# Kernel tuning notes

Hardware: AMD Instinct MI355X
Metric: run time of the kernel (lower is better)

Reference implementation:

```python
import jax, jax.numpy as jnp
import numpy as np

NPOS_MAX = 24  # npos_max
B, HEADS, H, W, HEAD_DIM = 8, 12, 24, 24, 64
SEQ = H * W


def setup_inputs() -> dict:
    key = jax.random.key(0)
    k1, k2, k3, k4 = jax.random.split(key, 4)
    # pos_emb params are zeros in torch init; randomized here so outputs/grads are nontrivial
    return {
        "query": jax.random.normal(k1, (B, HEADS, SEQ, HEAD_DIM), jnp.float32) * 0.1,
        "attn_logits": jax.random.normal(k2, (B, HEADS, SEQ, SEQ), jnp.float32),
        "pos_emb_x": jax.random.normal(k3, (HEAD_DIM, NPOS_MAX), jnp.float32) * 0.02,
        "pos_emb_y": jax.random.normal(k4, (HEAD_DIM, NPOS_MAX), jnp.float32) * 0.02,
        "wx": jnp.float32(0.5),
    }


def _cope_unit(query, attn_logits, pos_emb):
    # query: [N, heads, L, d]; attn_logits: [N, heads, L, L]; pos_emb: [d, npos]
    gates = jax.nn.sigmoid(attn_logits)
    pos = jnp.flip(jnp.cumsum(jnp.flip(gates, -1), axis=-1), -1)
    pos = jnp.minimum(pos, NPOS_MAX - 1)
    pos_ceil = jnp.ceil(pos).astype(jnp.int32)
    pos_floor = jnp.floor(pos).astype(jnp.int32)
    logits_int = jnp.einsum("nhld,dp->nhlp", query, pos_emb)  # [N,heads,L,npos]
    logits_ceil = jnp.take_along_axis(logits_int, pos_ceil, axis=-1)
    logits_floor = jnp.take_along_axis(logits_int, pos_floor, axis=-1)
    w = pos - pos_floor
    return logits_ceil * w + logits_floor * (1.0 - w)  # [N,heads,L,L]


def _cdist(x):
    # x: [BH, N, D] -> pairwise Euclidean distances [BH, N, N] (torch.cdist p=2)
    sq = jnp.sum(x * x, axis=-1)  # [BH, N]
    d2 = sq[:, :, None] + sq[:, None, :] - 2.0 * jnp.einsum("bnd,bmd->bnm", x, x)
    d2 = jnp.maximum(d2, 0.0)
    # safe sqrt: zero (not nan) gradient at identical points, matching torch.cdist
    return jnp.where(d2 > 0, jnp.sqrt(jnp.where(d2 > 0, d2, 1.0)), 0.0)


def reference(query, attn_logits, pos_emb_x, pos_emb_y, wx):
    b, heads, seq, d = query.shape
    h = w = int(np.sqrt(seq))
    q = query.reshape(b, heads, h, w, d)
    # row/column query slices (match torch permutes + reshapes)
    q_x = q.transpose(0, 2, 1, 3, 4).reshape(b * h, heads, w, d)
    q_y = q.transpose(0, 3, 1, 2, 4).reshape(b * w, heads, h, d)

    # vectorized replacement for the nested gather loops
    a = attn_logits.reshape(b, heads, h, w, h, w)
    # attn_x[b,h,i,j,k] = a[b,h,i,j,i,k]  -> diagonal over axes (2,4)
    attn_x = jnp.diagonal(a, axis1=2, axis2=4).transpose(0, 1, 4, 2, 3)  # [B,heads,H,W,W]
    # attn_y[b,h,i,j,k] = a[b,h,j,i,k,i]  -> diagonal over axes (3,5)
    attn_y = jnp.diagonal(a, axis1=3, axis2=5).transpose(0, 1, 4, 2, 3)  # [B,heads,W,H,H]

    # NOTE: faithful to the source's reshape (no permute) of [B,heads,H,W,W] -> [B*H,heads,W,W]
    attn_x_flat = attn_x.reshape(b * h, heads, w, w)
    attn_y_flat = attn_y.reshape(b * w, heads, h, h)

    w_x = _cope_unit(q_x, attn_x_flat, pos_emb_x).reshape(b, h, heads, w, w)
    w_y = _cope_unit(q_y, attn_y_flat, pos_emb_y).reshape(b, w, heads, h, h)

    # get_pe: flatten to [B*heads, H*W, W] / [B*heads, H*W, H] and take pairwise dists
    pe_x_flat = w_x.transpose(0, 2, 1, 3, 4).reshape(b * heads, h * w, w)
    pe_y_flat = w_y.transpose(0, 2, 3, 1, 4).reshape(b * heads, h * w, h)
    pe_res_x = _cdist(pe_x_flat).reshape(b, heads, h * w, h * w)
    pe_res_y = _cdist(pe_y_flat).reshape(b, heads, h * w, h * w)

    return wx * pe_res_x + (1.0 - wx) * pe_res_y
```

## Files before the change

kernel.cpp:

```cpp
#include <hip/hip_runtime.h>
#include <math.h>

#define NH 12
#define S 576
#define DD 64
#define P 24
#define NROWS 55296
#define GELEMS ((long)NROWS * P)
#define PSTRIDE 32

typedef unsigned int uint;
typedef unsigned short ushort;
typedef __bf16 bf16x8 __attribute__((ext_vector_type(8)));
typedef float f32x4 __attribute__((ext_vector_type(4)));

__device__ __forceinline__ uint bf16hi_bits(float v) {
    const uint u = __float_as_uint(v);
    return u + 0x7FFFu + ((u >> 16) & 1u);
}

__global__ __launch_bounds__(256) void gather_kernel(
    const float* __restrict__ attn, float* __restrict__ gx, float* __restrict__ gy)
{
    __shared__ float rb[16][580];
    const int tid = threadIdx.x;
    const int r0 = blockIdx.x * 16;
    const int hd = blockIdx.y, bb = blockIdx.z;
    const float4* src = (const float4*)(attn + ((long)(bb * NH + hd) * S + r0) * S);
    #pragma unroll
    for (int it = 0; it < 9; ++it) {
        const int i = it * 256 + tid;
        const int row = i / 144, c4 = i % 144;
        *(float4*)&rb[row][c4 * 4] = src[i];
    }
    __syncthreads();
    #pragma unroll
    for (int t = 0; t < 3; ++t) {
        const int e = t * 256 + tid;
        const int row = e / 48, jj = e % 48;
        const int r = r0 + row;
        const int band = r / 24, off = r % 24;
        if (jj < 24) {
            gx[((long)((bb * 288 + hd * 24 + band) * 24 + off)) * 24 + jj] =
                rb[row][band * 24 + jj];
        } else {
            const int k = jj - 24;
            gy[((long)((bb * 288 + hd * 24 + off) * 24 + band)) * 24 + k] =
                rb[row][k * 24 + off];
        }
    }
}

__global__ __launch_bounds__(256) void cope_kernel(
    const float* __restrict__ q,
    const float* __restrict__ gx, const float* __restrict__ gy,
    const float* __restrict__ Ex, const float* __restrict__ Ey,
    __bf16* __restrict__ pxh, __bf16* __restrict__ pxl,
    __bf16* __restrict__ pyh, __bf16* __restrict__ pyl,
    float* __restrict__ sqx, float* __restrict__ sqy)
{
    __shared__ float Et[24][68];
    __shared__ float Lr[32][28];
    __shared__ float Wr[32][28];

    const int tid = threadIdx.x;
    const int rl = tid >> 3, j = tid & 7;
    const int gidx0 = blockIdx.x * 32;
    const bool is_y = gidx0 >= NROWS;
    const int gu = gidx0 - (is_y ? NROWS : 0) + rl;

    const int l  = gu % 24;
    const int t2 = gu / 24;
    const int h  = t2 % NH, n = t2 / NH;
    const int bq = n / 24, oq = n % 24;
    const int qr = is_y ? (l * 24 + oq) : (oq * 24 + l);
    const int g  = bq * NH + h;

    const float* E = is_y ? Ey : Ex;
    for (int i = tid; i < 1536; i += 256) {
        const int d = i / 24, p = i % 24;
        Et[p][d] = E[i];
    }
    __syncthreads();

    const float* qrow = q + ((long)g * S + qr) * DD;
    float a0 = 0.f, a1 = 0.f, a2 = 0.f;
    const int p0 = j, p1 = j + 8, p2 = j + 16;
    #pragma unroll
    for (int d4 = 0; d4 < DD; d4 += 4) {
        const float4 qv = *(const float4*)(qrow + d4);
        const float4 e0 = *(const float4*)&Et[p0][d4];
        const float4 e1 = *(const float4*)&Et[p1][d4];
        const float4 e2 = *(const float4*)&Et[p2][d4];
        a0 = fmaf(qv.x, e0.x, fmaf(qv.y, e0.y, fmaf(qv.z, e0.z, fmaf(qv.w, e0.w, a0))));
        a1 = fmaf(qv.x, e1.x, fmaf(qv.y, e1.y, fmaf(qv.z, e1.z, fmaf(qv.w, e1.w, a1))));
        a2 = fmaf(qv.x, e2.x, fmaf(qv.y, e2.y, fmaf(qv.z, e2.z, fmaf(qv.w, e2.w, a2))));
    }
    Lr[rl][p0] = a0; Lr[rl][p1] = a1; Lr[rl][p2] = a2;
    __syncthreads();

    const float* grow = (is_y ? gy : gx) + (long)gu * P + 3 * j;
    float g0 = grow[0], g1 = grow[1], g2 = grow[2];
    g0 = 1.0f / (1.0f + __expf(-g0));
    g1 = 1.0f / (1.0f + __expf(-g1));
    g2 = 1.0f / (1.0f + __expf(-g2));
    const float s = g0 + g1 + g2;
    float T = s;
    #pragma unroll
    for (int d = 1; d < 8; d <<= 1) {
        const float o = __shfl_down(T, d, 8);
        T += (j + d < 8) ? o : 0.0f;
    }
    const float Exc = T - s;
    float posv[3];
    posv[0] = T;
    posv[1] = g1 + g2 + Exc;
    posv[2] = g2 + Exc;

    float sqp = 0.f;
    #pragma unroll
    for (int m = 0; m < 3; ++m) {
        const float pk  = fminf(posv[m], 23.0f);
        const float pf  = floorf(pk);
        const int   ic  = (int)ceilf(pk);
        const int   ifl = (int)pf;
        const float w   = pk - pf;
        const float o   = Lr[rl][ic] * w + Lr[rl][ifl] * (1.0f - w);
        Wr[rl][3 * j + m] = o;
        sqp += o * o;
    }
    #pragma unroll
    for (int d = 1; d < 8; d <<= 1) {
        const float o = __shfl_down(sqp, d, 8);
        sqp += (j + d < 8) ? o : 0.0f;
    }
    if (j == 0) (is_y ? sqy : sqx)[(long)g * S + qr] = sqp;
    __syncthreads();

    const int hl = tid >> 7, rem = tid & 127;
    const int r3 = rem >> 2, seg = rem & 3;
    const int gu3 = gidx0 - (is_y ? NROWS : 0) + r3;
    const int l3 = gu3 % 24, t23 = gu3 / 24;
    const int h3 = t23 % NH, n3 = t23 / NH;
    const int bq3 = n3 / 24, oq3 = n3 % 24;
    const int qr3 = is_y ? (l3 * 24 + oq3) : (oq3 * 24 + l3);
    const int g3 = bq3 * NH + h3;
    __bf16* dst = (is_y ? (hl ? pyl : pyh) : (hl ? pxl : pxh))
                  + ((long)g3 * S + qr3) * PSTRIDE + seg * 8;
    uint pk4[4] = {0u, 0u, 0u, 0u};
    if (seg < 3) {
        ushort hv[8];
        #pragma unroll
        for (int t = 0; t < 8; ++t) {
            const float o = Wr[r3][seg * 8 + t];
            const uint rh = bf16hi_bits(o);
            if (hl == 0) {
                hv[t] = (ushort)(rh >> 16);
            } else {
                const float hif = __uint_as_float(rh & 0xFFFF0000u);
                hv[t] = (ushort)(bf16hi_bits(o - hif) >> 16);
            }
        }
        #pragma unroll
        for (int t = 0; t < 4; ++t)
            pk4[t] = (uint)hv[2 * t] | ((uint)hv[2 * t + 1] << 16);
    }
    *(uint4*)dst = make_uint4(pk4[0], pk4[1], pk4[2], pk4[3]);
}

__global__ __launch_bounds__(256) void dist_kernel(
    const __bf16* __restrict__ pxh, const __bf16* __restrict__ pxl,
    const __bf16* __restrict__ pyh, const __bf16* __restrict__ pyl,
    const float* __restrict__ sqx, const float* __restrict__ sqy,
    const float* __restrict__ wxp, float* __restrict__ out)
{
    const int tid = threadIdx.x;
    const int w = tid >> 6, lane = tid & 63;
    const int til = blockIdx.x * 4 + w;
    if (til >= 81) return;
    const int g = blockIdx.y;
    const int tn = til / 9, tm = til % 9;
    const int lm = lane & 15, kg = lane >> 4;
    const float wx = wxp[0], wyc = 1.0f - wx;
    const long gb = (long)g * S;

    bf16x8 xbh[4], xbl[4], ybh[4], ybl[4];
    float smx[4], smy[4];
    #pragma unroll
    for (int nt = 0; nt < 4; ++nt) {
        const int row = tm * 64 + nt * 16 + lm;
        const long rb = (gb + row) * PSTRIDE + kg * 8;
        xbh[nt] = *(const bf16x8*)(pxh + rb);
        xbl[nt] = *(const bf16x8*)(pxl + rb);
        ybh[nt] = *(const bf16x8*)(pyh + rb);
        ybl[nt] = *(const bf16x8*)(pyl + rb);
        smx[nt] = sqx[gb + row];
        smy[nt] = sqy[gb + row];
    }

    #pragma unroll
    for (int mt = 0; mt < 4; ++mt) {
        const int arow = tn * 64 + mt * 16 + lm;
        const long ra = (gb + arow) * PSTRIDE + kg * 8;
        const bf16x8 xah = *(const bf16x8*)(pxh + ra);
        const bf16x8 xal = *(const bf16x8*)(pxl + ra);
        const bf16x8 yah = *(const bf16x8*)(pyh + ra);
        const bf16x8 yal = *(const bf16x8*)(pyl + ra);
        float snx[4], sny[4];
        #pragma unroll
        for (int rg = 0; rg < 4; ++rg) {
            const int r = tn * 64 + mt * 16 + kg * 4 + rg;
            snx[rg] = sqx[gb + r];
            sny[rg] = sqy[gb + r];
        }
        #pragma unroll
        for (int nt = 0; nt < 4; ++nt) {
            f32x4 ax = {0.f, 0.f, 0.f, 0.f};
            ax = __builtin_amdgcn_mfma_f32_16x16x32_bf16(xah, xbh[nt], ax, 0, 0, 0);
            ax = __builtin_amdgcn_mfma_f32_16x16x32_bf16(xah, xbl[nt], ax, 0, 0, 0);
            ax = __builtin_amdgcn_mfma_f32_16x16x32_bf16(xal, xbh[nt], ax, 0, 0, 0);
            f32x4 ay = {0.f, 0.f, 0.f, 0.f};
            ay = __builtin_amdgcn_mfma_f32_16x16x32_bf16(yah, ybh[nt], ay, 0, 0, 0);
            ay = __builtin_amdgcn_mfma_f32_16x16x32_bf16(yah, ybl[nt], ay, 0, 0, 0);
            ay = __builtin_amdgcn_mfma_f32_16x16x32_bf16(yal, ybh[nt], ay, 0, 0, 0);
            #pragma unroll
            for (int rg = 0; rg < 4; ++rg) {
                const int row = tn * 64 + mt * 16 + kg * 4 + rg;
                const int col = tm * 64 + nt * 16 + lm;
                const float d2x = fmaxf(fmaf(-2.0f, ax[rg], snx[rg] + smx[nt]), 0.0f);
                const float d2y = fmaxf(fmaf(-2.0f, ay[rg], sny[rg] + smy[nt]), 0.0f);
                const float dx = __builtin_amdgcn_sqrtf(d2x);
                const float dy = __builtin_amdgcn_sqrtf(d2y);
                out[(gb + row) * S + col] = fmaf(wx, dx, wyc * dy);
            }
        }
    }
}

extern "C" void kernel_launch(void* const* d_in, const int* in_sizes, int n_in,
                              void* d_out, int out_size, void* d_ws, size_t ws_size,
                              hipStream_t stream) {
    const float* q    = (const float*)d_in[0];
    const float* attn = (const float*)d_in[1];
    const float* Ex   = (const float*)d_in[2];
    const float* Ey   = (const float*)d_in[3];
    const float* wxp  = (const float*)d_in[4];
    float* out = (float*)d_out;

    float* gx = (float*)d_ws;
    float* gy = gx + GELEMS;
    __bf16* pxh = (__bf16*)(gy + GELEMS);
    __bf16* pxl = pxh + (long)NROWS * PSTRIDE;
    __bf16* pyh = pxl + (long)NROWS * PSTRIDE;
    __bf16* pyl = pyh + (long)NROWS * PSTRIDE;
    float* sqx = (float*)(pyl + (long)NROWS * PSTRIDE);
    float* sqy = sqx + NROWS;

    gather_kernel<<<dim3(36, NH, 8), 256, 0, stream>>>(attn, gx, gy);
    cope_kernel<<<3456, 256, 0, stream>>>(q, gx, gy, Ex, Ey,
                                          pxh, pxl, pyh, pyl, sqx, sqy);
    dist_kernel<<<dim3(21, 96), 256, 0, stream>>>(pxh, pxl, pyh, pyl,
                                                  sqx, sqy, wxp, out);
}
```

Before: 281.2 us.

## Fuse attention-logit gather into CoPE kernel, dropping gx/gy intermediates

Removes the separate gather kernel and its gx/gy workspace buffers. The CoPE kernel now loads a 24-row band of attention logits per block, extracts the x and y diagonal gates into shared memory, and handles 24 x-rows plus 24 y-rows per block with 384 threads. This saves one launch and a global write/read round trip of the gathered gates, but makes the gather's index mapping more intricate. The remapping of which rows each block owns must stay exactly equivalent to the original layout.

```diff
diff --git a/kernel.cpp b/kernel.cpp
--- a/kernel.cpp
+++ b/kernel.cpp
@@ -6,7 +6,6 @@
 #define DD 64
 #define P 24
 #define NROWS 55296
-#define GELEMS ((long)NROWS * P)
 #define PSTRIDE 32
 
 typedef unsigned int uint;
@@ -19,69 +18,55 @@
     return u + 0x7FFFu + ((u >> 16) & 1u);
 }
 
-__global__ __launch_bounds__(256) void gather_kernel(
-    const float* __restrict__ attn, float* __restrict__ gx, float* __restrict__ gy)
-{
-    __shared__ float rb[16][580];
-    const int tid = threadIdx.x;
-    const int r0 = blockIdx.x * 16;
-    const int hd = blockIdx.y, bb = blockIdx.z;
-    const float4* src = (const float4*)(attn + ((long)(bb * NH + hd) * S + r0) * S);
-    #pragma unroll
-    for (int it = 0; it < 9; ++it) {
-        const int i = it * 256 + tid;
-        const int row = i / 144, c4 = i % 144;
-        *(float4*)&rb[row][c4 * 4] = src[i];
-    }
-    __syncthreads();
-    #pragma unroll
-    for (int t = 0; t < 3; ++t) {
-        const int e = t * 256 + tid;
-        const int row = e / 48, jj = e % 48;
-        const int r = r0 + row;
-        const int band = r / 24, off = r % 24;
-        if (jj < 24) {
-            gx[((long)((bb * 288 + hd * 24 + band) * 24 + off)) * 24 + jj] =
-                rb[row][band * 24 + jj];
-        } else {
-            const int k = jj - 24;
-            gy[((long)((bb * 288 + hd * 24 + off) * 24 + band)) * 24 + k] =
-                rb[row][k * 24 + off];
-        }
-    }
-}
-
-__global__ __launch_bounds__(256) void cope_kernel(
+__global__ __launch_bounds__(384) void cope_fused_kernel(
     const float* __restrict__ q,
-    const float* __restrict__ gx, const float* __restrict__ gy,
+    const float* __restrict__ attn,
     const float* __restrict__ Ex, const float* __restrict__ Ey,
     __bf16* __restrict__ pxh, __bf16* __restrict__ pxl,
     __bf16* __restrict__ pyh, __bf16* __restrict__ pyl,
     float* __restrict__ sqx, float* __restrict__ sqy)
 {
-    __shared__ float Et[24][68];
-    __shared__ float Lr[32][28];
-    __shared__ float Wr[32][28];
+    __shared__ float Et[2][24][68];
+    __shared__ float xg[24][28];
+    __shared__ float yg[24][25];
+    __shared__ float Lr[48][28];
+    __shared__ float Wr[48][28];
 
     const int tid = threadIdx.x;
+    const int J = blockIdx.x, hd = blockIdx.y, b = blockIdx.z;
+
+    for (int i = tid; i < 3072; i += 384) {
+        const int u = i / 1536, r = i % 1536;
+        Et[u][r % 24][r / 24] = (u ? Ey : Ex)[r];
+    }
+
+    const float4* src = (const float4*)(attn + (((long)(b * NH + hd) * S + J * 24) * S));
+    const int c4lo = 6 * J;
+    #pragma unroll
+    for (int t = 0; t < 9; ++t) {
+        const int i = t * 384 + tid;
+        const int rr = i / 144, c4 = i % 144;
+        const float4 v = src[i];
+        if (c4 >= c4lo && c4 < c4lo + 6) {
+            *(float4*)&xg[rr][(c4 - c4lo) * 4] = v;
+        }
+        const int rem = (c4 * 4) % 24;
+        const int u = (rr - rem + 24) % 24;
+        if (u < 4) {
+            const float sel = (u == 0) ? v.x : (u == 1) ? v.y : (u == 2) ? v.z : v.w;
+            yg[rr][(c4 * 4 + u) / 24] = sel;
+        }
+    }
+    __syncthreads();
+
     const int rl = tid >> 3, j = tid & 7;
-    const int gidx0 = blockIdx.x * 32;
-    const bool is_y = gidx0 >= NROWS;
-    const int gu = gidx0 - (is_y ? NROWS : 0) + rl;
-
-    const int l  = gu % 24;
-    const int t2 = gu / 24;
-    const int h  = t2 % NH, n = t2 / NH;
-    const int bq = n / 24, oq = n % 24;
-    const int qr = is_y ? (l * 24 + oq) : (oq * 24 + l);
-    const int g  = bq * NH + h;
-
-    const float* E = is_y ? Ey : Ex;
-    for (int i = tid; i < 1536; i += 256) {
-        const int d = i / 24, p = i % 24;
-        Et[p][d] = E[i];
-    }
-    __syncthreads();
+    const bool is_y = rl >= 24;
+    const int rr = is_y ? rl - 24 : rl;
+    const int hq = is_y ? (rr % 12) : (J % 12);
+    const int oq = 2 * hd + (is_y ? rr / 12 : J / 12);
+    const int qr = is_y ? (J * 24 + oq) : (oq * 24 + rr);
+    const int g  = b * NH + hq;
+    const int eu = is_y ? 1 : 0;
 
     const float* qrow = q + ((long)g * S + qr) * DD;
     float a0 = 0.f, a1 = 0.f, a2 = 0.f;
@@ -89,9 +74,9 @@
     #pragma unroll
     for (int d4 = 0; d4 < DD; d4 += 4) {
         const float4 qv = *(const float4*)(qrow + d4);
-        const float4 e0 = *(const float4*)&Et[p0][d4];
-        const float4 e1 = *(const float4*)&Et[p1][d4];
-        const float4 e2 = *(const float4*)&Et[p2][d4];
+        const float4 e0 = *(const float4*)&Et[eu][p0][d4];
+        const float4 e1 = *(const float4*)&Et[eu][p1][d4];
+        const float4 e2 = *(const float4*)&Et[eu][p2][d4];
         a0 = fmaf(qv.x, e0.x, fmaf(qv.y, e0.y, fmaf(qv.z, e0.z, fmaf(qv.w, e0.w, a0))));
         a1 = fmaf(qv.x, e1.x, fmaf(qv.y, e1.y, fmaf(qv.z, e1.z, fmaf(qv.w, e1.w, a1))));
         a2 = fmaf(qv.x, e2.x, fmaf(qv.y, e2.y, fmaf(qv.z, e2.z, fmaf(qv.w, e2.w, a2))));
@@ -99,7 +84,7 @@
     Lr[rl][p0] = a0; Lr[rl][p1] = a1; Lr[rl][p2] = a2;
     __syncthreads();
 
-    const float* grow = (is_y ? gy : gx) + (long)gu * P + 3 * j;
+    const float* grow = (is_y ? &yg[rr][0] : &xg[rr][0]) + 3 * j;
     float g0 = grow[0], g1 = grow[1], g2 = grow[2];
     g0 = 1.0f / (1.0f + __expf(-g0));
     g1 = 1.0f / (1.0f + __expf(-g1));
@@ -137,15 +122,15 @@
     if (j == 0) (is_y ? sqy : sqx)[(long)g * S + qr] = sqp;
     __syncthreads();
 
-    const int hl = tid >> 7, rem = tid & 127;
-    const int r3 = rem >> 2, seg = rem & 3;
-    const int gu3 = gidx0 - (is_y ? NROWS : 0) + r3;
-    const int l3 = gu3 % 24, t23 = gu3 / 24;
-    const int h3 = t23 % NH, n3 = t23 / NH;
-    const int bq3 = n3 / 24, oq3 = n3 % 24;
-    const int qr3 = is_y ? (l3 * 24 + oq3) : (oq3 * 24 + l3);
-    const int g3 = bq3 * NH + h3;
-    __bf16* dst = (is_y ? (hl ? pyl : pyh) : (hl ? pxl : pxh))
+    const int hl = tid / 192, rem3 = tid % 192;
+    const int r3 = rem3 >> 2, seg = rem3 & 3;
+    const bool isy3 = r3 >= 24;
+    const int rr3 = isy3 ? r3 - 24 : r3;
+    const int hq3 = isy3 ? (rr3 % 12) : (J % 12);
+    const int oq3 = 2 * hd + (isy3 ? rr3 / 12 : J / 12);
+    const int qr3 = isy3 ? (J * 24 + oq3) : (oq3 * 24 + rr3);
+    const int g3 = b * NH + hq3;
+    __bf16* dst = (isy3 ? (hl ? pyl : pyh) : (hl ? pxl : pxh))
                   + ((long)g3 * S + qr3) * PSTRIDE + seg * 8;
     uint pk4[4] = {0u, 0u, 0u, 0u};
     if (seg < 3) {
@@ -247,18 +232,15 @@
     const float* wxp  = (const float*)d_in[4];
     float* out = (float*)d_out;
 
-    float* gx = (float*)d_ws;
-    float* gy = gx + GELEMS;
-    __bf16* pxh = (__bf16*)(gy + GELEMS);
+    __bf16* pxh = (__bf16*)d_ws;
     __bf16* pxl = pxh + (long)NROWS * PSTRIDE;
     __bf16* pyh = pxl + (long)NROWS * PSTRIDE;
     __bf16* pyl = pyh + (long)NROWS * PSTRIDE;
     float* sqx = (float*)(pyl + (long)NROWS * PSTRIDE);
     float* sqy = sqx + NROWS;
 
-    gather_kernel<<<dim3(36, NH, 8), 256, 0, stream>>>(attn, gx, gy);
-    cope_kernel<<<3456, 256, 0, stream>>>(q, gx, gy, Ex, Ey,
-                                          pxh, pxl, pyh, pyl, sqx, sqy);
+    cope_fused_kernel<<<dim3(24, NH, 8), 384, 0, stream>>>(
+        q, attn, Ex, Ey, pxh, pxl, pyh, pyl, sqx, sqy);
     dist_kernel<<<dim3(21, 96), 256, 0, stream>>>(pxh, pxl, pyh, pyl,
                                                   sqx, sqy, wxp, out);
 }
```

Result: no change. 279.5 us (-0.6%).
